# Performance work log

Hardware: AMD Instinct MI355X
Metric: run time of the kernel (lower is better)

The kernel has to match this reference:

```python
import jax, jax.numpy as jnp
import numpy as np

EMB = 64
N_NODES = 50000
N_EDGES = 800000

def _mlp(h, W1, b1, W2, b2):
    h = jax.nn.relu(h @ W1 + b1)
    return jax.nn.relu(h @ W2 + b2)

def setup_inputs() -> dict:
    key = jax.random.key(0)
    ks = jax.random.split(key, 12)
    s = 1.0 / np.sqrt(3 * EMB)
    s2 = 1.0 / np.sqrt(EMB)
    x = jax.random.normal(ks[0], (N_NODES, 2 * EMB), dtype=jnp.float32)
    edge_index = jax.random.randint(ks[1], (2, N_EDGES), 0, N_NODES, dtype=jnp.int32)
    edge_attr = jax.random.normal(ks[2], (N_EDGES, EMB), dtype=jnp.float32)
    u = jax.random.normal(ks[3], (64, 64), dtype=jnp.float32)
    batch = jax.random.randint(ks[4], (N_NODES,), 0, 64, dtype=jnp.int32)
    W1a = jax.random.uniform(ks[5], (3 * EMB, EMB), jnp.float32, -s, s)
    b1a = jax.random.uniform(ks[6], (EMB,), jnp.float32, -s, s)
    W1b = jax.random.uniform(ks[7], (EMB, EMB), jnp.float32, -s2, s2)
    b1b = jax.random.uniform(ks[8], (EMB,), jnp.float32, -s2, s2)
    W2a = jax.random.uniform(ks[9], (3 * EMB, EMB), jnp.float32, -s, s)
    b2a = jax.random.uniform(ks[10], (EMB,), jnp.float32, -s, s)
    W2b = jax.random.uniform(ks[11], (EMB, EMB), jnp.float32, -s2, s2)
    b2b = jax.random.uniform(jax.random.fold_in(key, 99), (EMB,), jnp.float32, -s2, s2)
    return {"x": x, "edge_index": edge_index, "edge_attr": edge_attr, "u": u, "batch": batch,
            "W1a": W1a, "b1a": b1a, "W1b": W1b, "b1b": b1b,
            "W2a": W2a, "b2a": b2a, "W2b": W2b, "b2b": b2b}

def reference(x, edge_index, edge_attr, u, batch, W1a, b1a, W1b, b1b, W2a, b2a, W2b, b2b):
    senders, receivers = edge_index[0], edge_index[1]
    # gather sender node features [E, 2*EMB] and concat edge features -> [E, 3*EMB]
    msg = jnp.concatenate([x[senders], edge_attr], axis=1)
    msg = _mlp(msg, W1a, b1a, W1b, b1b)  # [E, EMB]
    agg = jax.ops.segment_sum(msg, receivers, num_segments=x.shape[0])  # [N, EMB]
    h = jnp.concatenate([x, agg], axis=1)  # [N, 3*EMB]
    return _mlp(h, W2a, b2a, W2b, b2b)  # [N, EMB]
```

## Files before the change

kernel.cpp:

```cpp
#include <hip/hip_runtime.h>
#include <hip/hip_bf16.h>

typedef __attribute__((ext_vector_type(8))) __bf16 bf16x8;
typedef __attribute__((ext_vector_type(4))) float f32x4;

#define MFMA(a, b, c) __builtin_amdgcn_mfma_f32_16x16x32_bf16((a), (b), (c), 0, 0, 0)

__device__ __forceinline__ bf16x8 cvt8(const float* __restrict__ p) {
    const f32x4 a = *(const f32x4*)(p);
    const f32x4 b = *(const f32x4*)(p + 4);
    bf16x8 r;
    r[0] = (__bf16)a[0]; r[1] = (__bf16)a[1]; r[2] = (__bf16)a[2]; r[3] = (__bf16)a[3];
    r[4] = (__bf16)b[0]; r[5] = (__bf16)b[1]; r[6] = (__bf16)b[2]; r[7] = (__bf16)b[3];
    return r;
}

__global__ __launch_bounds__(256) void precompute_y(
    const float* __restrict__ x,
    const float* __restrict__ W1a, const float* __restrict__ b1a,
    const float* __restrict__ W2a, const float* __restrict__ b2a,
    float* __restrict__ y1, float* __restrict__ y2,
    int N, int ntiles)
{
    const int LDK = 136;
    __shared__ __align__(16) __bf16 w1t[64 * 136];
    __shared__ __align__(16) __bf16 w2t[64 * 136];
    for (int idx = threadIdx.x; idx < 64 * 128; idx += 256) {
        int k = idx >> 6, n = idx & 63;
        w1t[n * LDK + k] = (__bf16)W1a[k * 64 + n];
        w2t[n * LDK + k] = (__bf16)W2a[k * 64 + n];
    }
    __syncthreads();

    const int lane = threadIdx.x & 63, wave = threadIdx.x >> 6;
    const int l15 = lane & 15, l4 = lane >> 4;

    float bias1[4], bias2[4];
#pragma unroll
    for (int nt = 0; nt < 4; ++nt) {
        bias1[nt] = b1a[l15 + 16 * nt];
        bias2[nt] = b2a[l15 + 16 * nt];
    }

    for (int tile = blockIdx.x * 4 + wave; tile < ntiles; tile += gridDim.x * 4) {
        const int rbase = tile * 16;
        const int arow = min(rbase + l15, N - 1);
        f32x4 acc1[4], acc2[4];
#pragma unroll
        for (int nt = 0; nt < 4; ++nt) {
            acc1[nt] = (f32x4){0.f, 0.f, 0.f, 0.f};
            acc2[nt] = (f32x4){0.f, 0.f, 0.f, 0.f};
        }
#pragma unroll
        for (int j = 0; j < 4; ++j) {
            const int k0 = j * 32 + l4 * 8;
            bf16x8 a = cvt8(x + (size_t)arow * 128 + k0);
#pragma unroll
            for (int nt = 0; nt < 4; ++nt) {
                bf16x8 b1 = *(const bf16x8*)(w1t + (l15 + 16 * nt) * LDK + k0);
                acc1[nt] = MFMA(a, b1, acc1[nt]);
                bf16x8 b2 = *(const bf16x8*)(w2t + (l15 + 16 * nt) * LDK + k0);
                acc2[nt] = MFMA(a, b2, acc2[nt]);
            }
        }
#pragma unroll
        for (int nt = 0; nt < 4; ++nt) {
            const int col = l15 + 16 * nt;
#pragma unroll
            for (int r = 0; r < 4; ++r) {
                const int row = rbase + l4 * 4 + r;
                if (row < N) {
                    y1[(size_t)row * 64 + col] = acc1[nt][r] + bias1[nt];
                    y2[(size_t)row * 64 + col] = acc2[nt][r] + bias2[nt];
                }
            }
        }
    }
}

__global__ __launch_bounds__(256) void edge_pass(
    const float* __restrict__ eattr,
    const int* __restrict__ send, const int* __restrict__ recv,
    const float* __restrict__ W1a, const float* __restrict__ W1b,
    const float* __restrict__ b1b,
    const float* __restrict__ y1, float* __restrict__ agg,
    int E, int ntiles)
{
    const int LDK = 72;
    __shared__ __align__(16) __bf16 wat[64 * 72];
    __shared__ __align__(16) __bf16 wbt[64 * 72];
    __shared__ __align__(16) __bf16 hbuf[4][16 * 72];
    for (int idx = threadIdx.x; idx < 64 * 64; idx += 256) {
        int k = idx >> 6, n = idx & 63;
        wat[n * LDK + k] = (__bf16)W1a[(128 + k) * 64 + n];
        wbt[n * LDK + k] = (__bf16)W1b[k * 64 + n];
    }
    __syncthreads();

    const int lane = threadIdx.x & 63, wave = threadIdx.x >> 6;
    const int l15 = lane & 15, l4 = lane >> 4;
    __bf16* hb = hbuf[wave];

    float biasb[4];
#pragma unroll
    for (int nt = 0; nt < 4; ++nt) biasb[nt] = b1b[l15 + 16 * nt];

    for (int tile = blockIdx.x * 4 + wave; tile < ntiles; tile += gridDim.x * 4) {
        const int ebase = tile * 16;

        f32x4 acc[4];
        int rcv[4];
#pragma unroll
        for (int r = 0; r < 4; ++r) {
            const int e = min(ebase + l4 * 4 + r, E - 1);
            const int s = send[e];
            rcv[r] = recv[e];
            const float* yp = y1 + (size_t)s * 64 + l15;
#pragma unroll
            for (int nt = 0; nt < 4; ++nt) acc[nt][r] = yp[16 * nt];
        }
        const int arow = min(ebase + l15, E - 1);
#pragma unroll
        for (int j = 0; j < 2; ++j) {
            const int k0 = j * 32 + l4 * 8;
            bf16x8 a = cvt8(eattr + (size_t)arow * 64 + k0);
#pragma unroll
            for (int nt = 0; nt < 4; ++nt) {
                bf16x8 b = *(const bf16x8*)(wat + (l15 + 16 * nt) * LDK + k0);
                acc[nt] = MFMA(a, b, acc[nt]);
            }
        }
#pragma unroll
        for (int nt = 0; nt < 4; ++nt)
#pragma unroll
            for (int r = 0; r < 4; ++r)
                hb[(l4 * 4 + r) * LDK + (l15 + 16 * nt)] = (__bf16)fmaxf(acc[nt][r], 0.f);

        f32x4 acc2[4];
#pragma unroll
        for (int nt = 0; nt < 4; ++nt)
            acc2[nt] = (f32x4){biasb[nt], biasb[nt], biasb[nt], biasb[nt]};
#pragma unroll
        for (int j = 0; j < 2; ++j) {
            const int k0 = j * 32 + l4 * 8;
            bf16x8 a = *(const bf16x8*)(hb + l15 * LDK + k0);
#pragma unroll
            for (int nt = 0; nt < 4; ++nt) {
                bf16x8 b = *(const bf16x8*)(wbt + (l15 + 16 * nt) * LDK + k0);
                acc2[nt] = MFMA(a, b, acc2[nt]);
            }
        }
#pragma unroll
        for (int nt = 0; nt < 4; ++nt) {
            const int col = l15 + 16 * nt;
#pragma unroll
            for (int r = 0; r < 4; ++r) {
                const int e = ebase + l4 * 4 + r;
                if (e < E)
                    atomicAdd(agg + (size_t)rcv[r] * 64 + col, fmaxf(acc2[nt][r], 0.f));
            }
        }
    }
}

__global__ __launch_bounds__(256) void node_pass(
    const float* __restrict__ agg,
    const float* __restrict__ W2a, const float* __restrict__ W2b,
    const float* __restrict__ b2b,
    const float* __restrict__ y2, float* __restrict__ out,
    int N, int ntiles)
{
    const int LDK = 72;
    __shared__ __align__(16) __bf16 wat[64 * 72];
    __shared__ __align__(16) __bf16 wbt[64 * 72];
    __shared__ __align__(16) __bf16 hbuf[4][16 * 72];
    for (int idx = threadIdx.x; idx < 64 * 64; idx += 256) {
        int k = idx >> 6, n = idx & 63;
        wat[n * LDK + k] = (__bf16)W2a[(128 + k) * 64 + n];
        wbt[n * LDK + k] = (__bf16)W2b[k * 64 + n];
    }
    __syncthreads();

    const int lane = threadIdx.x & 63, wave = threadIdx.x >> 6;
    const int l15 = lane & 15, l4 = lane >> 4;
    __bf16* hb = hbuf[wave];

    float biasb[4];
#pragma unroll
    for (int nt = 0; nt < 4; ++nt) biasb[nt] = b2b[l15 + 16 * nt];

    for (int tile = blockIdx.x * 4 + wave; tile < ntiles; tile += gridDim.x * 4) {
        const int rbase = tile * 16;

        f32x4 acc[4];
#pragma unroll
        for (int r = 0; r < 4; ++r) {
            const int row = min(rbase + l4 * 4 + r, N - 1);
            const float* yp = y2 + (size_t)row * 64 + l15;
#pragma unroll
            for (int nt = 0; nt < 4; ++nt) acc[nt][r] = yp[16 * nt];
        }
        const int arow = min(rbase + l15, N - 1);
#pragma unroll
        for (int j = 0; j < 2; ++j) {
            const int k0 = j * 32 + l4 * 8;
            bf16x8 a = cvt8(agg + (size_t)arow * 64 + k0);
#pragma unroll
            for (int nt = 0; nt < 4; ++nt) {
                bf16x8 b = *(const bf16x8*)(wat + (l15 + 16 * nt) * LDK + k0);
                acc[nt] = MFMA(a, b, acc[nt]);
            }
        }
#pragma unroll
        for (int nt = 0; nt < 4; ++nt)
#pragma unroll
            for (int r = 0; r < 4; ++r)
                hb[(l4 * 4 + r) * LDK + (l15 + 16 * nt)] = (__bf16)fmaxf(acc[nt][r], 0.f);

        f32x4 acc2[4];
#pragma unroll
        for (int nt = 0; nt < 4; ++nt)
            acc2[nt] = (f32x4){biasb[nt], biasb[nt], biasb[nt], biasb[nt]};
#pragma unroll
        for (int j = 0; j < 2; ++j) {
            const int k0 = j * 32 + l4 * 8;
            bf16x8 a = *(const bf16x8*)(hb + l15 * LDK + k0);
#pragma unroll
            for (int nt = 0; nt < 4; ++nt) {
                bf16x8 b = *(const bf16x8*)(wbt + (l15 + 16 * nt) * LDK + k0);
                acc2[nt] = MFMA(a, b, acc2[nt]);
            }
        }
#pragma unroll
        for (int nt = 0; nt < 4; ++nt) {
            const int col = l15 + 16 * nt;
#pragma unroll
            for (int r = 0; r < 4; ++r) {
                const int row = rbase + l4 * 4 + r;
                if (row < N)
                    out[(size_t)row * 64 + col] = fmaxf(acc2[nt][r], 0.f);
            }
        }
    }
}

extern "C" void kernel_launch(void* const* d_in, const int* in_sizes, int n_in,
                              void* d_out, int out_size, void* d_ws, size_t ws_size,
                              hipStream_t stream) {
    const float* x     = (const float*)d_in[0];
    const int*   eidx  = (const int*)d_in[1];
    const float* eattr = (const float*)d_in[2];
    const float* W1a = (const float*)d_in[5];
    const float* b1a = (const float*)d_in[6];
    const float* W1b = (const float*)d_in[7];
    const float* b1b = (const float*)d_in[8];
    const float* W2a = (const float*)d_in[9];
    const float* b2a = (const float*)d_in[10];
    const float* W2b = (const float*)d_in[11];
    const float* b2b = (const float*)d_in[12];
    float* out = (float*)d_out;

    const int N = in_sizes[0] / 128;
    const int E = in_sizes[1] / 2;
    const int* send = eidx;
    const int* recv = eidx + E;

    float* agg = (float*)d_ws;
    float* y1  = agg + (size_t)N * 64;
    float* y2  = y1 + (size_t)N * 64;

    hipMemsetAsync(agg, 0, (size_t)N * 64 * sizeof(float), stream);

    const int ntilesN = (N + 15) / 16;
    const int ntilesE = (E + 15) / 16;
    const int blkN = (ntilesN + 3) / 4;
    int blkE = (ntilesE + 3) / 4;
    if (blkE > 2048) blkE = 2048;

    precompute_y<<<blkN, 256, 0, stream>>>(x, W1a, b1a, W2a, b2a, y1, y2, N, ntilesN);
    edge_pass<<<blkE, 256, 0, stream>>>(eattr, send, recv, W1a, W1b, b1b, y1, agg, E, ntilesE);
    node_pass<<<blkN, 256, 0, stream>>>(agg, W2a, W2b, b2b, y2, out, N, ntilesN);
}
```

Before: 216.4 us.

## Transpose MFMA operands so each lane owns one row, enabling vector loads/atomics

```diff
diff --git a/kernel.cpp b/kernel.cpp
--- a/kernel.cpp
+++ b/kernel.cpp
@@ -2,7 +2,9 @@
 #include <hip/hip_bf16.h>
 
 typedef __attribute__((ext_vector_type(8))) __bf16 bf16x8;
+typedef __attribute__((ext_vector_type(4))) __bf16 bf16x4;
 typedef __attribute__((ext_vector_type(4))) float f32x4;
+typedef __attribute__((ext_vector_type(2))) float f32x2;
 
 #define MFMA(a, b, c) __builtin_amdgcn_mfma_f32_16x16x32_bf16((a), (b), (c), 0, 0, 0)
 
@@ -13,6 +15,17 @@
     r[0] = (__bf16)a[0]; r[1] = (__bf16)a[1]; r[2] = (__bf16)a[2]; r[3] = (__bf16)a[3];
     r[4] = (__bf16)b[0]; r[5] = (__bf16)b[1]; r[6] = (__bf16)b[2]; r[7] = (__bf16)b[3];
     return r;
+}
+
+__device__ __forceinline__ void atom2(float* p, float a, float b) {
+#if __has_builtin(__builtin_amdgcn_global_atomic_fadd_v2f32)
+    typedef f32x2 __attribute__((address_space(1)))* gp2;
+    f32x2 v = {a, b};
+    __builtin_amdgcn_global_atomic_fadd_v2f32((gp2)(unsigned long long)p, v);
+#else
+    unsafeAtomicAdd(p, a);
+    unsafeAtomicAdd(p + 1, b);
+#endif
 }
 
 __global__ __launch_bounds__(256) void precompute_y(
@@ -35,16 +48,16 @@
     const int lane = threadIdx.x & 63, wave = threadIdx.x >> 6;
     const int l15 = lane & 15, l4 = lane >> 4;
 
-    float bias1[4], bias2[4];
+    f32x4 bias1[4], bias2[4];
 #pragma unroll
     for (int nt = 0; nt < 4; ++nt) {
-        bias1[nt] = b1a[l15 + 16 * nt];
-        bias2[nt] = b2a[l15 + 16 * nt];
+        bias1[nt] = *(const f32x4*)(b1a + nt * 16 + l4 * 4);
+        bias2[nt] = *(const f32x4*)(b2a + nt * 16 + l4 * 4);
     }
 
     for (int tile = blockIdx.x * 4 + wave; tile < ntiles; tile += gridDim.x * 4) {
-        const int rbase = tile * 16;
-        const int arow = min(rbase + l15, N - 1);
+        const int node = tile * 16 + l15;
+        const int nrow = min(node, N - 1);
         f32x4 acc1[4], acc2[4];
 #pragma unroll
         for (int nt = 0; nt < 4; ++nt) {
@@ -54,25 +67,22 @@
 #pragma unroll
         for (int j = 0; j < 4; ++j) {
             const int k0 = j * 32 + l4 * 8;
-            bf16x8 a = cvt8(x + (size_t)arow * 128 + k0);
-#pragma unroll
-            for (int nt = 0; nt < 4; ++nt) {
-                bf16x8 b1 = *(const bf16x8*)(w1t + (l15 + 16 * nt) * LDK + k0);
-                acc1[nt] = MFMA(a, b1, acc1[nt]);
-                bf16x8 b2 = *(const bf16x8*)(w2t + (l15 + 16 * nt) * LDK + k0);
-                acc2[nt] = MFMA(a, b2, acc2[nt]);
-            }
-        }
-#pragma unroll
-        for (int nt = 0; nt < 4; ++nt) {
-            const int col = l15 + 16 * nt;
-#pragma unroll
-            for (int r = 0; r < 4; ++r) {
-                const int row = rbase + l4 * 4 + r;
-                if (row < N) {
-                    y1[(size_t)row * 64 + col] = acc1[nt][r] + bias1[nt];
-                    y2[(size_t)row * 64 + col] = acc2[nt][r] + bias2[nt];
-                }
+            bf16x8 b = cvt8(x + (size_t)nrow * 128 + k0);
+#pragma unroll
+            for (int nt = 0; nt < 4; ++nt) {
+                bf16x8 a1 = *(const bf16x8*)(w1t + (nt * 16 + l15) * LDK + k0);
+                acc1[nt] = MFMA(a1, b, acc1[nt]);
+                bf16x8 a2 = *(const bf16x8*)(w2t + (nt * 16 + l15) * LDK + k0);
+                acc2[nt] = MFMA(a2, b, acc2[nt]);
+            }
+        }
+        if (node < N) {
+#pragma unroll
+            for (int nt = 0; nt < 4; ++nt) {
+                f32x4 v1 = acc1[nt] + bias1[nt];
+                f32x4 v2 = acc2[nt] + bias2[nt];
+                *(f32x4*)(y1 + (size_t)node * 64 + nt * 16 + l4 * 4) = v1;
+                *(f32x4*)(y2 + (size_t)node * 64 + nt * 16 + l4 * 4) = v2;
             }
         }
     }
@@ -101,63 +111,61 @@
     const int l15 = lane & 15, l4 = lane >> 4;
     __bf16* hb = hbuf[wave];
 
-    float biasb[4];
-#pragma unroll
-    for (int nt = 0; nt < 4; ++nt) biasb[nt] = b1b[l15 + 16 * nt];
+    f32x4 biasb[4];
+#pragma unroll
+    for (int nt = 0; nt < 4; ++nt) biasb[nt] = *(const f32x4*)(b1b + nt * 16 + l4 * 4);
 
     for (int tile = blockIdx.x * 4 + wave; tile < ntiles; tile += gridDim.x * 4) {
-        const int ebase = tile * 16;
+        const int e = tile * 16 + l15;
+        const int eload = min(e, E - 1);
+        const int s  = send[eload];
+        const int rv = recv[eload];
 
         f32x4 acc[4];
-        int rcv[4];
-#pragma unroll
-        for (int r = 0; r < 4; ++r) {
-            const int e = min(ebase + l4 * 4 + r, E - 1);
-            const int s = send[e];
-            rcv[r] = recv[e];
-            const float* yp = y1 + (size_t)s * 64 + l15;
-#pragma unroll
-            for (int nt = 0; nt < 4; ++nt) acc[nt][r] = yp[16 * nt];
-        }
-        const int arow = min(ebase + l15, E - 1);
-#pragma unroll
-        for (int j = 0; j < 2; ++j) {
-            const int k0 = j * 32 + l4 * 8;
-            bf16x8 a = cvt8(eattr + (size_t)arow * 64 + k0);
-#pragma unroll
-            for (int nt = 0; nt < 4; ++nt) {
-                bf16x8 b = *(const bf16x8*)(wat + (l15 + 16 * nt) * LDK + k0);
+#pragma unroll
+        for (int nt = 0; nt < 4; ++nt)
+            acc[nt] = *(const f32x4*)(y1 + (size_t)s * 64 + nt * 16 + l4 * 4);
+#pragma unroll
+        for (int j = 0; j < 2; ++j) {
+            const int k0 = j * 32 + l4 * 8;
+            bf16x8 b = cvt8(eattr + (size_t)eload * 64 + k0);
+#pragma unroll
+            for (int nt = 0; nt < 4; ++nt) {
+                bf16x8 a = *(const bf16x8*)(wat + (nt * 16 + l15) * LDK + k0);
                 acc[nt] = MFMA(a, b, acc[nt]);
             }
         }
 #pragma unroll
-        for (int nt = 0; nt < 4; ++nt)
-#pragma unroll
-            for (int r = 0; r < 4; ++r)
-                hb[(l4 * 4 + r) * LDK + (l15 + 16 * nt)] = (__bf16)fmaxf(acc[nt][r], 0.f);
+        for (int nt = 0; nt < 4; ++nt) {
+            bf16x4 hv;
+#pragma unroll
+            for (int r = 0; r < 4; ++r) hv[r] = (__bf16)fmaxf(acc[nt][r], 0.f);
+            *(bf16x4*)(hb + l15 * LDK + nt * 16 + l4 * 4) = hv;
+        }
 
         f32x4 acc2[4];
 #pragma unroll
-        for (int nt = 0; nt < 4; ++nt)
-            acc2[nt] = (f32x4){biasb[nt], biasb[nt], biasb[nt], biasb[nt]};
-#pragma unroll
-        for (int j = 0; j < 2; ++j) {
-            const int k0 = j * 32 + l4 * 8;
-            bf16x8 a = *(const bf16x8*)(hb + l15 * LDK + k0);
-#pragma unroll
-            for (int nt = 0; nt < 4; ++nt) {
-                bf16x8 b = *(const bf16x8*)(wbt + (l15 + 16 * nt) * LDK + k0);
+        for (int nt = 0; nt < 4; ++nt) acc2[nt] = biasb[nt];
+#pragma unroll
+        for (int j = 0; j < 2; ++j) {
+            const int k0 = j * 32 + l4 * 8;
+            bf16x8 b = *(const bf16x8*)(hb + l15 * LDK + k0);
+#pragma unroll
+            for (int nt = 0; nt < 4; ++nt) {
+                bf16x8 a = *(const bf16x8*)(wbt + (nt * 16 + l15) * LDK + k0);
                 acc2[nt] = MFMA(a, b, acc2[nt]);
             }
         }
-#pragma unroll
-        for (int nt = 0; nt < 4; ++nt) {
-            const int col = l15 + 16 * nt;
-#pragma unroll
-            for (int r = 0; r < 4; ++r) {
-                const int e = ebase + l4 * 4 + r;
-                if (e < E)
-                    atomicAdd(agg + (size_t)rcv[r] * 64 + col, fmaxf(acc2[nt][r], 0.f));
+        if (e < E) {
+            float* base = agg + (size_t)rv * 64;
+#pragma unroll
+            for (int nt = 0; nt < 4; ++nt) {
+                float v0 = fmaxf(acc2[nt][0], 0.f);
+                float v1 = fmaxf(acc2[nt][1], 0.f);
+                float v2 = fmaxf(acc2[nt][2], 0.f);
+                float v3 = fmaxf(acc2[nt][3], 0.f);
+                atom2(base + nt * 16 + l4 * 4, v0, v1);
+                atom2(base + nt * 16 + l4 * 4 + 2, v2, v3);
             }
         }
     }
@@ -185,60 +193,56 @@
     const int l15 = lane & 15, l4 = lane >> 4;
     __bf16* hb = hbuf[wave];
 
-    float biasb[4];
-#pragma unroll
-    for (int nt = 0; nt < 4; ++nt) biasb[nt] = b2b[l15 + 16 * nt];
+    f32x4 biasb[4];
+#pragma unroll
+    for (int nt = 0; nt < 4; ++nt) biasb[nt] = *(const f32x4*)(b2b + nt * 16 + l4 * 4);
 
     for (int tile = blockIdx.x * 4 + wave; tile < ntiles; tile += gridDim.x * 4) {
-        const int rbase = tile * 16;
+        const int node = tile * 16 + l15;
+        const int nrow = min(node, N - 1);
 
         f32x4 acc[4];
 #pragma unroll
-        for (int r = 0; r < 4; ++r) {
-            const int row = min(rbase + l4 * 4 + r, N - 1);
-            const float* yp = y2 + (size_t)row * 64 + l15;
-#pragma unroll
-            for (int nt = 0; nt < 4; ++nt) acc[nt][r] = yp[16 * nt];
-        }
-        const int arow = min(rbase + l15, N - 1);
-#pragma unroll
-        for (int j = 0; j < 2; ++j) {
-            const int k0 = j * 32 + l4 * 8;
-            bf16x8 a = cvt8(agg + (size_t)arow * 64 + k0);
-#pragma unroll
-            for (int nt = 0; nt < 4; ++nt) {
-                bf16x8 b = *(const bf16x8*)(wat + (l15 + 16 * nt) * LDK + k0);
+        for (int nt = 0; nt < 4; ++nt)
+            acc[nt] = *(const f32x4*)(y2 + (size_t)nrow * 64 + nt * 16 + l4 * 4);
+#pragma unroll
+        for (int j = 0; j < 2; ++j) {
+            const int k0 = j * 32 + l4 * 8;
+            bf16x8 b = cvt8(agg + (size_t)nrow * 64 + k0);
+#pragma unroll
+            for (int nt = 0; nt < 4; ++nt) {
+                bf16x8 a = *(const bf16x8*)(wat + (nt * 16 + l15) * LDK + k0);
                 acc[nt] = MFMA(a, b, acc[nt]);
             }
         }
 #pragma unroll
-        for (int nt = 0; nt < 4; ++nt)
-#pragma unroll
-            for (int r = 0; r < 4; ++r)
-                hb[(l4 * 4 + r) * LDK + (l15 + 16 * nt)] = (__bf16)fmaxf(acc[nt][r], 0.f);
+        for (int nt = 0; nt < 4; ++nt) {
+            bf16x4 hv;
+#pragma unroll
+            for (int r = 0; r < 4; ++r) hv[r] = (__bf16)fmaxf(acc[nt][r], 0.f);
+            *(bf16x4*)(hb + l15 * LDK + nt * 16 + l4 * 4) = hv;
+        }
 
         f32x4 acc2[4];
 #pragma unroll
-        for (int nt = 0; nt < 4; ++nt)
-            acc2[nt] = (f32x4){biasb[nt], biasb[nt], biasb[nt], biasb[nt]};
-#pragma unroll
-        for (int j = 0; j < 2; ++j) {
-            const int k0 = j * 32 + l4 * 8;
-            bf16x8 a = *(const bf16x8*)(hb + l15 * LDK + k0);
-#pragma unroll
-            for (int nt = 0; nt < 4; ++nt) {
-                bf16x8 b = *(const bf16x8*)(wbt + (l15 + 16 * nt) * LDK + k0);
+        for (int nt = 0; nt < 4; ++nt) acc2[nt] = biasb[nt];
+#pragma unroll
+        for (int j = 0; j < 2; ++j) {
+            const int k0 = j * 32 + l4 * 8;
+            bf16x8 b = *(const bf16x8*)(hb + l15 * LDK + k0);
+#pragma unroll
+            for (int nt = 0; nt < 4; ++nt) {
+                bf16x8 a = *(const bf16x8*)(wbt + (nt * 16 + l15) * LDK + k0);
                 acc2[nt] = MFMA(a, b, acc2[nt]);
             }
         }
-#pragma unroll
-        for (int nt = 0; nt < 4; ++nt) {
-            const int col = l15 + 16 * nt;
-#pragma unroll
-            for (int r = 0; r < 4; ++r) {
-                const int row = rbase + l4 * 4 + r;
-                if (row < N)
-                    out[(size_t)row * 64 + col] = fmaxf(acc2[nt][r], 0.f);
+        if (node < N) {
+#pragma unroll
+            for (int nt = 0; nt < 4; ++nt) {
+                f32x4 v;
+#pragma unroll
+                for (int r = 0; r < 4; ++r) v[r] = fmaxf(acc2[nt][r], 0.f);
+                *(f32x4*)(out + (size_t)node * 64 + nt * 16 + l4 * 4) = v;
             }
         }
     }
@@ -273,9 +277,10 @@
 
     const int ntilesN = (N + 15) / 16;
     const int ntilesE = (E + 15) / 16;
-    const int blkN = (ntilesN + 3) / 4;
+    int blkN = (ntilesN + 3) / 4;
+    if (blkN > 1024) blkN = 1024;
     int blkE = (ntilesE + 3) / 4;
-    if (blkE > 2048) blkE = 2048;
+    if (blkE > 1280) blkE = 1280;
 
     precompute_y<<<blkN, 256, 0, stream>>>(x, W1a, b1a, W2a, b2a, y1, y2, N, ntilesN);
     edge_pass<<<blkE, 256, 0, stream>>>(eattr, send, recv, W1a, W1b, b1b, y1, agg, E, ntilesE);
```

New measurement: 727.6 us. 3.36x slower.
